# Kernel tuning notes

Measured on AMD Instinct MI355X. Metric: run time of the kernel, lower is better.

The kernel has to match this reference:

```python
import jax, jax.numpy as jnp
import numpy as np

VOXEL_SIZE = jnp.array([0.075, 0.075], dtype=jnp.float32)
PC_RANGE = jnp.array([-54.0, -54.0], dtype=jnp.float32)
FUSION_STRIDE = 8.0
SRC_STRIDES = (4.0, 8.0)
RADII = (2.4, 4.8)
NSAMPLE = 16
NKEY = 500


def _mlp(x, w1, g1, b1, w2, b2):
    # Linear(no bias) + BatchNorm(eval, running mean=0/var=1 -> affine) + ReLU, then Linear
    h = jax.nn.relu((x @ w1) * g1 + b1)
    return h @ w2 + b2


def _world(coords, stride):
    # voxel coord -> world xy center
    return (coords.astype(jnp.float32) + 0.5) * stride * VOXEL_SIZE + PC_RANGE


def _gather_rows(x, idx):
    # x: (B, N, ...), idx: (B, ...) -> per-batch row gather
    return jax.vmap(lambda f, i: f[i])(x, idx)


def _knn(key_world, src_world, src_feat, radius):
    # key_world (B,Nk,2), src_world (B,Ns,2), src_feat (B,Ns,C)
    d2 = jnp.sum((key_world[:, :, None, :] - src_world[:, None, :, :]) ** 2, axis=-1)  # (B,Nk,Ns)
    d2 = jnp.where(d2 <= radius * radius, d2, jnp.inf)
    negd, idx = jax.lax.top_k(-d2, NSAMPLE)  # nearest NSAMPLE within radius, (B,Nk,K)
    valid = jnp.isfinite(negd).astype(src_feat.dtype)  # empty==0 mask
    feats = _gather_rows(src_feat, idx)  # (B,Nk,K,C)
    return feats * valid[..., None]


def setup_inputs() -> dict:
    key = jax.random.key(0)
    ks = jax.random.split(key, 24)
    s = 0.05
    return {
        'fusion_feat': jax.random.normal(ks[0], (2, 20000, 128), jnp.float32),
        'src_feat_a': jax.random.normal(ks[1], (2, 30000, 128), jnp.float32),
        'src_feat_b': jax.random.normal(ks[2], (2, 30000, 128), jnp.float32),
        'heat_w1': jax.random.normal(ks[3], (128, 128), jnp.float32) * s,
        'heat_g1': jnp.ones((128,), jnp.float32),
        'heat_b1': jnp.zeros((128,), jnp.float32),
        'heat_w2': jax.random.normal(ks[4], (128, 10), jnp.float32) * s,
        'heat_b2': jnp.zeros((10,), jnp.float32),
        'knn_w': jax.random.normal(ks[5], (2, 16), jnp.float32) * s,
        'knn_b': jnp.zeros((2,), jnp.float32),
        'kw_w1': jax.random.normal(ks[6], (128, 64), jnp.float32) * s,
        'kw_g1': jnp.ones((64,), jnp.float32),
        'kw_b1': jnp.zeros((64,), jnp.float32),
        'kw_w2': jax.random.normal(ks[7], (64, 3), jnp.float32) * s,
        'kw_b2': jnp.zeros((3,), jnp.float32),
        'fuse_w1': jax.random.normal(ks[8], (256, 256), jnp.float32) * s,
        'fuse_g1': jnp.ones((256,), jnp.float32),
        'fuse_b1': jnp.zeros((256,), jnp.float32),
        'fuse_w2': jax.random.normal(ks[9], (256, 128), jnp.float32) * s,
        'fuse_b2': jnp.zeros((128,), jnp.float32),
        'fusion_coords': jax.random.randint(ks[10], (2, 20000, 2), 0, 180, jnp.int32),
        'src_coords_a': jax.random.randint(ks[11], (2, 30000, 2), 0, 360, jnp.int32),
        'src_coords_b': jax.random.randint(ks[12], (2, 30000, 2), 0, 180, jnp.int32),
    }


def reference(fusion_feat, src_feat_a, src_feat_b, heat_w1, heat_g1, heat_b1,
              heat_w2, heat_b2, knn_w, knn_b, kw_w1, kw_g1, kw_b1, kw_w2, kw_b2,
              fuse_w1, fuse_g1, fuse_b1, fuse_w2, fuse_b2,
              fusion_coords, src_coords_a, src_coords_b):
    B = fusion_feat.shape[0]
    # heatmap head over all fusion voxels
    scores10 = _mlp(fusion_feat, heat_w1, heat_g1, heat_b1, heat_w2, heat_b2)  # (B,Nf,10)
    heat_scores = jnp.max(scores10, axis=-1)
    cls = jnp.argmax(scores10, axis=-1)
    # per-sample top-k key voxel selection
    _, tki = jax.lax.top_k(jax.nn.sigmoid(heat_scores), NKEY)  # (B,Nk)
    key_feat = _gather_rows(fusion_feat, tki)      # (B,Nk,128)
    key_coords = _gather_rows(fusion_coords, tki)  # (B,Nk,2)
    key_class = _gather_rows(cls, tki)             # (B,Nk)
    key_world = _world(key_coords, FUSION_STRIDE)  # (B,Nk,2)

    srcs = ((src_feat_a, src_coords_a), (src_feat_b, src_coords_b))
    mlp_feats = []
    for s, (sf, sc) in enumerate(srcs):
        sw = _world(sc, SRC_STRIDES[s])
        kf = _knn(key_world, sw, sf, RADII[s])  # (B,Nk,K,C), zeroed where empty
        # Linear over the K neighbor axis (knn_feat_mlp: NSAMPLE -> 1)
        mf = jnp.einsum('bnkc,k->bnc', kf, knn_w[s]) + knn_b[s]
        mlp_feats.append(mf)

    w = jax.nn.softmax(_mlp(key_feat, kw_w1, kw_g1, kw_b1, kw_w2, kw_b2), axis=-1)  # (B,Nk,3)
    # faithful to original: key_voxel_feat is re-scaled cumulatively inside the loop
    kvf = key_feat
    fuse_sum = jnp.zeros_like(key_feat)
    for i in range(len(srcs)):
        kvf = w[..., i:i + 1] * kvf
        fuse_sum = fuse_sum + kvf * mlp_feats[i]
    fused = jnp.concatenate([fuse_sum, kvf], axis=-1)  # (B,Nk,256)
    out = _mlp(fused, fuse_w1, fuse_g1, fuse_b1, fuse_w2, fuse_b2)  # (B,Nk,128)

    bs_col = jnp.broadcast_to(jnp.arange(B, dtype=key_coords.dtype)[:, None, None], (B, NKEY, 1))
    key_voxel_indices = jnp.concatenate([bs_col, key_coords], axis=-1).reshape(B * NKEY, 3)
    return (out.reshape(B * NKEY, -1), key_voxel_indices,
            heat_scores.reshape(-1), scores10.reshape(-1, scores10.shape[-1]), key_class)
```

## Files before the change

### kernel.cpp

```cpp
#include <hip/hip_runtime.h>
#include <math.h>

#define BB 2
#define NF 20000
#define NS 30000
#define CH 128
#define NK 500
#define KNN 16
#define KPB 4

#define HA 2.4024f
#define HB 4.8048f
#define NCA 45
#define NCB 23
#define CELLS_A 2025
#define CELLS_B 529

#define GB 8
#define SLICE 3750
#define SLICE4 1875

#define OUT0_OFF 0
#define OUT1_OFF 128000
#define OUT2_OFF 131000
#define OUT3_OFF 171000
#define OUT4_OFF 571000

#define WS_CLS   0
#define WS_TKI   160000
#define WS_KW    164000
#define WS_MF    172000
#define WS_KEYS  WS_MF
#define WS_BH    492000
#define WS_GSTART 1196000
#define WS_PTS    1236880
#define WS_PIDX   2196880

#define STB(s,b)  ((s) ? (4052 + (b) * 530) : ((b) * 2026))

__device__ __forceinline__ void fma4(float4& acc, float sc, const float4& wv) {
    acc.x += sc * wv.x; acc.y += sc * wv.y;
    acc.z += sc * wv.z; acc.w += sc * wv.w;
}

__device__ __forceinline__ unsigned ordf(float s) {
    unsigned u = __float_as_uint(s);
    return (u & 0x80000000u) ? ~u : (u | 0x80000000u);
}

__device__ __forceinline__ int cell_of(int cxi, int cyi, float stride, float inv_h,
                                       int nc, float& sx, float& sy)
{
    sx = __fadd_rn(__fmul_rn(__fmul_rn(__fadd_rn((float)cxi, 0.5f), stride), 0.075f), -54.0f);
    sy = __fadd_rn(__fmul_rn(__fmul_rn(__fadd_rn((float)cyi, 0.5f), stride), 0.075f), -54.0f);
    int cx = (int)floorf((sx + 54.0f) * inv_h);
    int cy = (int)floorf((sy + 54.0f) * inv_h);
    cx = min(max(cx, 0), nc - 1);
    cy = min(max(cy, 0), nc - 1);
    return cy * nc + cx;
}

__global__ __launch_bounds__(256) void heat_kernel(
    const float* __restrict__ x,
    const float* __restrict__ w1,
    const float* __restrict__ g1, const float* __restrict__ b1,
    const float* __restrict__ w2,
    const float* __restrict__ b2,
    float* __restrict__ out_heat,
    float* __restrict__ out_s10,
    int* __restrict__ cls,
    unsigned long long* __restrict__ keys,
    const int* __restrict__ sca, const int* __restrict__ scb,
    int* __restrict__ bh)
{
    __shared__ float As[64 * 72];
    __shared__ float Ws[64 * 132];
    __shared__ float W2s[1280];
    const int tid = threadIdx.x;

    if (blockIdx.x < 4 * GB) {
        const int gflat = blockIdx.x;
        const int sb = gflat >> 3;
        const int gg = gflat & (GB - 1);
        const int s = sb >> 1, b = sb & 1;
        const float stride = s ? 8.0f : 4.0f;
        const float inv_h = s ? (1.0f / HB) : (1.0f / HA);
        const int nc = s ? NCB : NCA;
        const int2* sc = ((const int2*)(s ? scb : sca)) + (size_t)b * NS;
        const int4* scv = (const int4*)sc;
        int* hist = (int*)As;

        for (int i = tid; i < 2048; i += 256) hist[i] = 0;
        __syncthreads();
        for (int p = gg * SLICE4 + tid; p < (gg + 1) * SLICE4; p += 256) {
            int4 v = scv[p];
            float sx, sy;
            int cell0 = cell_of(v.x, v.y, stride, inv_h, nc, sx, sy);
            int cell1 = cell_of(v.z, v.w, stride, inv_h, nc, sx, sy);
            atomicAdd(&hist[cell0], 1);
            atomicAdd(&hist[cell1], 1);
        }
        __syncthreads();
        int* bhp = bh + (gflat << 11);
        for (int i = tid; i < 2048; i += 256) bhp[i] = hist[i];
        return;
    }

    const int m0 = (blockIdx.x - 4 * GB) * 64;
    const int tx = tid & 15;
    const int ty = tid >> 4;

    for (int v = tid; v < 1280; v += 256) W2s[v] = w2[v];

    float acc[4][8];
#pragma unroll
    for (int i = 0; i < 4; ++i)
#pragma unroll
        for (int j = 0; j < 8; ++j) acc[i][j] = 0.f;

    const float4* xv = (const float4*)x;
    const float4* w1v = (const float4*)w1;

    for (int kc = 0; kc < 128; kc += 64) {
#pragma unroll
        for (int i = 0; i < 4; ++i) {
            int v = tid + i * 256;
            int row = v >> 4, c4 = v & 15;
            float4 val = xv[(size_t)(m0 + row) * 32 + (kc >> 2) + c4];
            *(float4*)&As[row * 72 + c4 * 4] = val;
        }
#pragma unroll
        for (int i = 0; i < 8; ++i) {
            int v = tid + i * 256;
            int k = v >> 5, c4 = v & 31;
            float4 val = w1v[(size_t)(kc + k) * 32 + c4];
            *(float4*)&Ws[k * 132 + c4 * 4] = val;
        }
        __syncthreads();

        const float* a0p = &As[(ty * 4 + 0) * 72];
        const float* a1p = &As[(ty * 4 + 1) * 72];
        const float* a2p = &As[(ty * 4 + 2) * 72];
        const float* a3p = &As[(ty * 4 + 3) * 72];
#pragma unroll 4
        for (int k = 0; k < 64; ++k) {
            float4 bA = *(const float4*)&Ws[k * 132 + tx * 8];
            float4 bB = *(const float4*)&Ws[k * 132 + tx * 8 + 4];
            float a0 = a0p[k], a1 = a1p[k], a2 = a2p[k], a3 = a3p[k];
            acc[0][0] += a0 * bA.x; acc[0][1] += a0 * bA.y; acc[0][2] += a0 * bA.z; acc[0][3] += a0 * bA.w;
            acc[0][4] += a0 * bB.x; acc[0][5] += a0 * bB.y; acc[0][6] += a0 * bB.z; acc[0][7] += a0 * bB.w;
            acc[1][0] += a1 * bA.x; acc[1][1] += a1 * bA.y; acc[1][2] += a1 * bA.z; acc[1][3] += a1 * bA.w;
            acc[1][4] += a1 * bB.x; acc[1][5] += a1 * bB.y; acc[1][6] += a1 * bB.z; acc[1][7] += a1 * bB.w;
            acc[2][0] += a2 * bA.x; acc[2][1] += a2 * bA.y; acc[2][2] += a2 * bA.z; acc[2][3] += a2 * bA.w;
            acc[2][4] += a2 * bB.x; acc[2][5] += a2 * bB.y; acc[2][6] += a2 * bB.z; acc[2][7] += a2 * bB.w;
            acc[3][0] += a3 * bA.x; acc[3][1] += a3 * bA.y; acc[3][2] += a3 * bA.z; acc[3][3] += a3 * bA.w;
            acc[3][4] += a3 * bB.x; acc[3][5] += a3 * bB.y; acc[3][6] += a3 * bB.z; acc[3][7] += a3 * bB.w;
        }
        __syncthreads();
    }

    float4 g1a = ((const float4*)g1)[tx * 2], g1b = ((const float4*)g1)[tx * 2 + 1];
    float4 b1a = ((const float4*)b1)[tx * 2], b1b = ((const float4*)b1)[tx * 2 + 1];
    float* Hs = Ws;
#pragma unroll
    for (int i = 0; i < 4; ++i) {
        int row = ty * 4 + i;
        float4 hA, hB;
        hA.x = fmaxf(acc[i][0] * g1a.x + b1a.x, 0.f);
        hA.y = fmaxf(acc[i][1] * g1a.y + b1a.y, 0.f);
        hA.z = fmaxf(acc[i][2] * g1a.z + b1a.z, 0.f);
        hA.w = fmaxf(acc[i][3] * g1a.w + b1a.w, 0.f);
        hB.x = fmaxf(acc[i][4] * g1b.x + b1b.x, 0.f);
        hB.y = fmaxf(acc[i][5] * g1b.y + b1b.y, 0.f);
        hB.z = fmaxf(acc[i][6] * g1b.z + b1b.z, 0.f);
        hB.w = fmaxf(acc[i][7] * g1b.w + b1b.w, 0.f);
        *(float4*)&Hs[row * 132 + tx * 8] = hA;
        *(float4*)&Hs[row * 132 + tx * 8 + 4] = hB;
    }
    __syncthreads();

    const int r = tid >> 2;
    const int p = tid & 3;
    float a2[10];
#pragma unroll
    for (int c = 0; c < 10; ++c) a2[c] = 0.f;
    for (int kk = 0; kk < 32; ++kk) {
        int k = kk * 4 + p;
        float hv = Hs[r * 132 + k];
#pragma unroll
        for (int c = 0; c < 10; ++c) a2[c] += hv * W2s[k * 10 + c];
    }
#pragma unroll
    for (int c = 0; c < 10; ++c) {
        a2[c] += __shfl_xor(a2[c], 1);
        a2[c] += __shfl_xor(a2[c], 2);
    }
    if (p == 0) {
        int m = m0 + r;
        float best = -INFINITY;
        int bi = 0;
#pragma unroll
        for (int c = 0; c < 10; ++c) {
            float s = a2[c] + b2[c];
            out_s10[(size_t)m * 10 + c] = s;
            if (s > best) { best = s; bi = c; }
        }
        out_heat[m] = best;
        cls[m] = bi;
        int b = m / NF;
        unsigned i = (unsigned)(m - b * NF);
        float sig = 1.0f / (1.0f + expf(-best));
        keys[m] = ((unsigned long long)ordf(sig) << 32) | (unsigned)(~i);
    }
}

#define H1BINS 16384

__global__ __launch_bounds__(1024) void mid_kernel(
    const unsigned long long* __restrict__ keys,
    const int* __restrict__ cls,
    const int* __restrict__ fcoords,
    float* __restrict__ out1,
    float* __restrict__ out4,
    int* __restrict__ tki,
    float* __restrict__ keyworld,
    const int* __restrict__ sca, const int* __restrict__ scb,
    const int* __restrict__ bh,
    int* __restrict__ gstart,
    float2* __restrict__ pts, int* __restrict__ pidx)
{
    __shared__ unsigned h[H1BINS];
    __shared__ unsigned sA[1024], sB[1024];
    __shared__ unsigned long long list[1024];
    __shared__ unsigned chunk_s, aboveC_s, T1_s, aboveT1_s, cand_s, thr_s, cnt_s;
    const int tid = threadIdx.x;
    const int blk = blockIdx.x;

    if (blk >= 2) {
        const int idx = blk - 2;
        const int sb = idx >> 3;
        const int j = idx & (GB - 1);
        const int s = sb >> 1, b = sb & 1;
        const int n = s ? CELLS_B : CELLS_A;
        const int nc = s ? NCB : NCA;
        const float stride = s ? 8.0f : 4.0f;
        const float inv_h = s ? (1.0f / HB) : (1.0f / HA);
        const int stb = STB(s, b);
        const int2* sc = ((const int2*)(s ? scb : sca)) + (size_t)b * NS;
        const int4* scv = (const int4*)sc;
        const size_t pbase = ((size_t)s * BB + b) * NS;
        const int* bhsb = bh + (sb << 14);
        int* tot = (int*)h;
        int* cur = ((int*)h) + 2048;
        int* scn0 = (int*)sA;
        int* scn1 = (int*)sB;

        for (int c = tid; c < 2048; c += 1024) {
            int t = 0, pr = 0;
#pragma unroll
            for (int g = 0; g < GB; ++g) {
                int v = bhsb[(g << 11) + c];
                t += v;
                if (g < j) pr += v;
            }
            tot[c] = t;
            cur[c] = pr;
        }
        __syncthreads();
        const int i0 = tid * 2, i1 = tid * 2 + 1;
        int c0 = (i0 < n) ? tot[i0] : 0;
        int c1 = (i1 < n) ? tot[i1] : 0;
        scn0[tid] = c0 + c1;
        __syncthreads();
        int* srcp = scn0; int* dstp = scn1;
        for (int off = 1; off < 1024; off <<= 1) {
            int v = srcp[tid];
            if (tid >= off) v += srcp[tid - off];
            dstp[tid] = v;
            __syncthreads();
            int* t = srcp; srcp = dstp; dstp = t;
        }
        const int excl = (tid == 0) ? 0 : srcp[tid - 1];
        if (i0 < n) {
            if (j == 0) gstart[stb + i0] = excl;
            cur[i0] += excl;
        }
        if (i1 < n) {
            if (j == 0) gstart[stb + i1] = excl + c0;
            cur[i1] += excl + c0;
        }
        if (j == 0 && tid == 0) gstart[stb + n] = NS;
        __syncthreads();
        for (int p = j * SLICE4 + tid; p < (j + 1) * SLICE4; p += 1024) {
            int4 v = scv[p];
            float sx0, sy0, sx1, sy1;
            int cell0 = cell_of(v.x, v.y, stride, inv_h, nc, sx0, sy0);
            int cell1 = cell_of(v.z, v.w, stride, inv_h, nc, sx1, sy1);
            int pos0 = atomicAdd(&cur[cell0], 1);
            int pos1 = atomicAdd(&cur[cell1], 1);
            pts[pbase + pos0] = make_float2(sx0, sy0);
            pidx[pbase + pos0] = p * 2;
            pts[pbase + pos1] = make_float2(sx1, sy1);
            pidx[pbase + pos1] = p * 2 + 1;
        }
        return;
    }

    const int b = blk;
    const unsigned long long* kb = keys + (size_t)b * NF;
    const unsigned K = NK;

    for (int i = tid; i < H1BINS; i += 1024) h[i] = 0u;
    __syncthreads();
#pragma unroll 4
    for (int i = tid; i < NF; i += 1024)
        atomicAdd(&h[(unsigned)(kb[i] >> 50)], 1u);
    __syncthreads();
    unsigned ck = 0;
    {
        int base = tid * 16;
#pragma unroll
        for (int j = 0; j < 16; ++j) ck += h[base + j];
        sA[tid] = ck;
    }
    __syncthreads();
    unsigned* srcp = sA; unsigned* dstp = sB;
    for (int off = 1; off < 1024; off <<= 1) {
        unsigned v = srcp[tid];
        if (tid + off < 1024) v += srcp[tid + off];
        dstp[tid] = v;
        __syncthreads();
        unsigned* t = srcp; srcp = dstp; dstp = t;
    }
    {
        unsigned suf = srcp[tid];
        unsigned above = suf - ck;
        if (above < K && K <= suf) { chunk_s = (unsigned)tid; aboveC_s = above; }
    }
    __syncthreads();
    if (tid == 0) {
        int bin = (int)chunk_s * 16 + 15;
        unsigned acc = aboveC_s;
        for (;; --bin) { if (acc + h[bin] >= K) break; acc += h[bin]; }
        T1_s = (unsigned)bin;
        aboveT1_s = acc;
        cand_s = acc + h[bin];
        cnt_s = 0u;
    }
    __syncthreads();
    const unsigned T1 = T1_s;

    if (cand_s <= 1024u) {
#pragma unroll 4
        for (int i = tid; i < NF; i += 1024) {
            unsigned long long key = kb[i];
            if ((unsigned)(key >> 50) >= T1) {
                unsigned pos = atomicAdd(&cnt_s, 1u);
                if (pos < 1024u) list[pos] = key;
            }
        }
    } else {
        const unsigned K2 = K - aboveT1_s;
        h[tid] = 0u;
        __syncthreads();
#pragma unroll 4
        for (int i = tid; i < NF; i += 1024) {
            unsigned long long key = kb[i];
            if ((unsigned)(key >> 50) == T1)
                atomicAdd(&h[(unsigned)(key >> 40) & 1023u], 1u);
        }
        __syncthreads();
        unsigned hb = h[tid];
        sA[tid] = hb;
        __syncthreads();
        unsigned* s2 = sA; unsigned* d2 = sB;
        for (int off = 1; off < 1024; off <<= 1) {
            unsigned v = s2[tid];
            if (tid + off < 1024) v += s2[tid + off];
            d2[tid] = v;
            __syncthreads();
            unsigned* t = s2; s2 = d2; d2 = t;
        }
        {
            unsigned suf = s2[tid];
            unsigned above = suf - hb;
            if (above < K2 && K2 <= suf) thr_s = (T1 << 10) | (unsigned)tid;
        }
        __syncthreads();
        const unsigned thr24 = thr_s;
#pragma unroll 4
        for (int i = tid; i < NF; i += 1024) {
            unsigned long long key = kb[i];
            if ((unsigned)(key >> 40) >= thr24) {
                unsigned pos = atomicAdd(&cnt_s, 1u);
                if (pos < 1024u) list[pos] = key;
            }
        }
    }
    __syncthreads();
    const int cc = (int)(cnt_s > 1024u ? 1024u : cnt_s);

    if (tid < cc) {
        unsigned long long mykey = list[tid];
        unsigned r = 0;
#pragma unroll 8
        for (int j = 0; j < cc; ++j) r += (list[j] > mykey) ? 1u : 0u;
        if (r < (unsigned)NK) {
            int idx = (int)(~(unsigned)(mykey & 0xFFFFFFFFull));
            tki[b * NK + (int)r] = idx;
            int c0 = fcoords[((size_t)b * NF + idx) * 2 + 0];
            int c1 = fcoords[((size_t)b * NF + idx) * 2 + 1];
            size_t o = (size_t)(b * NK + (int)r);
            out1[o * 3 + 0] = (float)b;
            out1[o * 3 + 1] = (float)c0;
            out1[o * 3 + 2] = (float)c1;
            float wx = __fadd_rn(__fmul_rn(__fmul_rn(__fadd_rn((float)c0, 0.5f), 8.0f), 0.075f), -54.0f);
            float wy = __fadd_rn(__fmul_rn(__fmul_rn(__fadd_rn((float)c1, 0.5f), 8.0f), 0.075f), -54.0f);
            keyworld[o * 2 + 0] = wx;
            keyworld[o * 2 + 1] = wy;
            out4[o] = (float)cls[(size_t)b * NF + idx];
        }
    }
}

__global__ __launch_bounds__(256) void knn_kernel(
    const float* __restrict__ sfa, const float* __restrict__ sfb,
    const int* __restrict__ gstart,
    const float2* __restrict__ pts, const int* __restrict__ pidx,
    const float* __restrict__ knn_w,
    const float* __restrict__ knn_b,
    const float* __restrict__ keyworld,
    float* __restrict__ mf)
{
    __shared__ unsigned long long list[1024];
    __shared__ float psum[128];
    __shared__ unsigned cnt_s;
    const int tid = threadIdx.x;
    const int blk = blockIdx.x;
    const int s = blk / (BB * NK);
    const int rest = blk % (BB * NK);
    const int b = rest / NK;
    const int r = rest % NK;
    const float* sfeat = s ? sfb : sfa;
    const float r2 = s ? (float)(4.8 * 4.8) : (float)(2.4 * 2.4);
    const float inv_h = s ? (1.0f / HB) : (1.0f / HA);
    const int nc = s ? NCB : NCA;
    const int stb = STB(s, b);
    const size_t pbase = ((size_t)s * BB + b) * NS;

    if (tid == 0) cnt_s = 0u;
    __syncthreads();
    const float kx = keyworld[((size_t)b * NK + r) * 2 + 0];
    const float ky = keyworld[((size_t)b * NK + r) * 2 + 1];
    int cx = (int)floorf((kx + 54.0f) * inv_h);
    int cy = (int)floorf((ky + 54.0f) * inv_h);
    cx = min(max(cx, 0), nc - 1);
    cy = min(max(cy, 0), nc - 1);
    const int c0 = max(cx - 1, 0), c1 = min(cx + 1, nc - 1);
    const int cy0 = max(cy - 1, 0), cy1 = min(cy + 1, nc - 1);

    for (int cyy = cy0; cyy <= cy1; ++cyy) {
        int lo = gstart[stb + cyy * nc + c0];
        int hi = gstart[stb + cyy * nc + c1 + 1];
        for (int p = lo + tid; p < hi; p += 256) {
            float2 w = pts[pbase + p];
            float dx = __fsub_rn(kx, w.x);
            float dy = __fsub_rn(ky, w.y);
            float d2 = __fadd_rn(__fmul_rn(dx, dx), __fmul_rn(dy, dy));
            if (d2 <= r2) {
                unsigned pos = atomicAdd(&cnt_s, 1u);
                if (pos < 1024u)
                    list[pos] = ((unsigned long long)__float_as_uint(d2) << 32)
                              | (unsigned)pidx[pbase + p];
            }
        }
    }
    __syncthreads();
    int cc = (int)cnt_s;
    if (cc > 1024) cc = 1024;
    int n2 = 16;
    while (n2 < cc) n2 <<= 1;
    for (int i = tid; i < n2; i += 256)
        if (i >= cc) list[i] = ~0ull;
    __syncthreads();
    for (int kk = 2; kk <= n2; kk <<= 1) {
        for (int j = kk >> 1; j > 0; j >>= 1) {
            for (int i = tid; i < n2; i += 256) {
                int ixj = i ^ j;
                if (ixj > i) {
                    unsigned long long a = list[i], bv = list[ixj];
                    bool up = ((i & kk) == 0);
                    bool sw = up ? (a > bv) : (a < bv);
                    if (sw) { list[i] = bv; list[ixj] = a; }
                }
            }
            __syncthreads();
        }
    }
    {
        int K = cc < KNN ? cc : KNN;
        int col = tid & 127, half = tid >> 7;
        float acc = 0.f;
        int k0 = half * 8, k1 = min(K, half * 8 + 8);
        for (int k = k0; k < k1; ++k) {
            unsigned i = (unsigned)(list[k] & 0xFFFFFFFFull);
            acc += knn_w[s * 16 + k] * sfeat[((size_t)b * NS + i) * CH + col];
        }
        if (half) psum[col] = acc;
        __syncthreads();
        if (!half)
            mf[(((size_t)s * BB + b) * NK + r) * CH + col] = knn_b[s] + acc + psum[col];
    }
}

__global__ __launch_bounds__(1024) void fuse_kernel(
    const float* __restrict__ ffeat,
    const int* __restrict__ tki,
    const float* __restrict__ kw_w1, const float* __restrict__ kw_g1,
    const float* __restrict__ kw_b1, const float* __restrict__ kw_w2,
    const float* __restrict__ kw_b2,
    const float* __restrict__ fuse_w1, const float* __restrict__ fuse_g1,
    const float* __restrict__ fuse_b1, const float* __restrict__ fuse_w2,
    const float* __restrict__ fuse_b2,
    const float* __restrict__ mf,
    float* __restrict__ out0)
{
    __shared__ float pL[16384];
    __shared__ float xsT[512];
    __shared__ float mfs[1024];
    __shared__ float fusedvT[1024];
    __shared__ float h2sT[1024];
    __shared__ float prm[964];
    __shared__ float hsX[256];
    __shared__ float p2[96];
    __shared__ float l3[12];
    __shared__ float wsm[8];
    __shared__ int idxs[KPB], bs[KPB], rs[KPB];
    const int tid = threadIdx.x;
    const int f0 = blockIdx.x * KPB;

    if (tid < 964) {
        float v;
        if (tid < 64)       v = kw_g1[tid];
        else if (tid < 128) v = kw_b1[tid - 64];
        else if (tid < 320) v = kw_w2[tid - 128];
        else if (tid < 323) v = kw_b2[tid - 320];
        else if (tid < 324) v = 0.f;
        else if (tid < 580) v = fuse_g1[tid - 324];
        else if (tid < 836) v = fuse_b1[tid - 580];
        else                v = fuse_b2[tid - 836];
        prm[tid] = v;
    }
    if (tid < KPB) {
        int flat = f0 + tid;
        int b = flat / NK;
        bs[tid] = b;
        rs[tid] = flat - b * NK;
        idxs[tid] = tki[flat];
    }
    __syncthreads();

    if (tid < 128) {
        int key = tid >> 5, c4 = tid & 31;
        float4 v = ((const float4*)(ffeat + ((size_t)bs[key] * NF + idxs[key]) * CH))[c4];
        xsT[(c4 * 4 + 0) * 4 + key] = v.x;
        xsT[(c4 * 4 + 1) * 4 + key] = v.y;
        xsT[(c4 * 4 + 2) * 4 + key] = v.z;
        xsT[(c4 * 4 + 3) * 4 + key] = v.w;
    }
    if (tid < 256) {
        int ss = tid >> 7, key = (tid >> 5) & 3, c4 = tid & 31;
        float4 v = ((const float4*)(mf + (((size_t)ss * BB + bs[key]) * NK + rs[key]) * CH))[c4];
        *(float4*)&mfs[ss * 512 + key * 128 + c4 * 4] = v;
    }
    __syncthreads();

    if (tid < 256) {
        const int og = tid & 15, kseg = tid >> 4;
        float4 wr[8];
#pragma unroll
        for (int m = 0; m < 8; ++m)
            wr[m] = ((const float4*)kw_w1)[(kseg * 8 + m) * 16 + og];
        float4 a0 = {0, 0, 0, 0}, a1 = {0, 0, 0, 0}, a2 = {0, 0, 0, 0}, a3 = {0, 0, 0, 0};
#pragma unroll
        for (int m = 0; m < 8; ++m) {
            float4 f4 = *(const float4*)&xsT[(kseg * 8 + m) * 4];
            fma4(a0, f4.x, wr[m]);
            fma4(a1, f4.y, wr[m]);
            fma4(a2, f4.z, wr[m]);
            fma4(a3, f4.w, wr[m]);
        }
        *(float4*)&pL[(kseg * 4 + 0) * 64 + og * 4] = a0;
        *(float4*)&pL[(kseg * 4 + 1) * 64 + og * 4] = a1;
        *(float4*)&pL[(kseg * 4 + 2) * 64 + og * 4] = a2;
        *(float4*)&pL[(kseg * 4 + 3) * 64 + og * 4] = a3;
    }
    __syncthreads();
    if (tid < 256) {
        int out = tid >> 2, key = tid & 3;
        float s = 0.f;
#pragma unroll
        for (int ks = 0; ks < 16; ++ks) s += pL[(ks * 4 + key) * 64 + out];
        float t = s * prm[out] + prm[64 + out];
        hsX[key * 64 + out] = t > 0.f ? t : 0.f;
    }
    __syncthreads();
    if (tid < 96) {
        int key = tid / 24, rr = tid % 24, out = rr >> 3, seg = rr & 7;
        float acc = 0.f;
#pragma unroll
        for (int m = 0; m < 8; ++m) {
            int k = seg * 8 + m;
            acc += hsX[key * 64 + k] * prm[128 + k * 3 + out];
        }
        p2[(key * 3 + out) * 8 + seg] = acc;
    }
    __syncthreads();
    if (tid < 12) {
        int key = tid / 3, out = tid % 3;
        float s = 0.f;
#pragma unroll
        for (int j = 0; j < 8; ++j) s += p2[(key * 3 + out) * 8 + j];
        l3[key * 3 + out] = s + prm[320 + out];
    }
    __syncthreads();
    if (tid < KPB) {
        float l0 = l3[tid * 3], l1 = l3[tid * 3 + 1], l2 = l3[tid * 3 + 2];
        float m = fmaxf(l0, fmaxf(l1, l2));
        float e0 = expf(l0 - m), e1 = expf(l1 - m), e2 = expf(l2 - m);
        float sum = e0 + e1 + e2;
        wsm[tid * 2 + 0] = e0 / sum;
        wsm[tid * 2 + 1] = e1 / sum;
    }
    __syncthreads();

    {
        int c = tid >> 2, key = tid & 3;
        float w0 = wsm[key * 2], w1_ = wsm[key * 2 + 1];
        float val;
        if (c < 128) {
            float xv_ = xsT[c * 4 + key];
            float m0 = mfs[key * 128 + c];
            float m1 = mfs[512 + key * 128 + c];
            float kv = w0 * xv_;
            float kv2 = w1_ * kv;
            val = kv * m0 + kv2 * m1;
        } else {
            float xv_ = xsT[(c - 128) * 4 + key];
            val = w1_ * (w0 * xv_);
        }
        fusedvT[tid] = val;
    }
    __syncthreads();

    {
        const int og = tid & 63, kseg = tid >> 6;
        const float4* w1v = (const float4*)fuse_w1;
        float4 wr[16];
#pragma unroll
        for (int m = 0; m < 16; ++m)
            wr[m] = w1v[(kseg * 16 + m) * 64 + og];
        float4 a0 = {0, 0, 0, 0}, a1 = {0, 0, 0, 0}, a2 = {0, 0, 0, 0}, a3 = {0, 0, 0, 0};
#pragma unroll
        for (int m = 0; m < 16; ++m) {
            float4 f4 = *(const float4*)&fusedvT[(kseg * 16 + m) * 4];
            fma4(a0, f4.x, wr[m]);
            fma4(a1, f4.y, wr[m]);
            fma4(a2, f4.z, wr[m]);
            fma4(a3, f4.w, wr[m]);
        }
        *(float4*)&pL[(kseg * 4 + 0) * 256 + og * 4] = a0;
        *(float4*)&pL[(kseg * 4 + 1) * 256 + og * 4] = a1;
        *(float4*)&pL[(kseg * 4 + 2) * 256 + og * 4] = a2;
        *(float4*)&pL[(kseg * 4 + 3) * 256 + og * 4] = a3;
    }
    __syncthreads();
    {
        int out = tid >> 2, key = tid & 3;
        float s = 0.f;
#pragma unroll
        for (int ks = 0; ks < 16; ++ks) s += pL[(ks * 4 + key) * 256 + out];
        float t = s * prm[324 + out] + prm[580 + out];
        h2sT[out * 4 + key] = t > 0.f ? t : 0.f;
    }
    __syncthreads();

    {
        const int og2 = tid & 31, kseg2 = tid >> 5;
        const float4* w2v = (const float4*)fuse_w2;
        float4 wr[8];
#pragma unroll
        for (int m = 0; m < 8; ++m)
            wr[m] = w2v[(kseg2 * 8 + m) * 32 + og2];
        float4 a0 = {0, 0, 0, 0}, a1 = {0, 0, 0, 0}, a2 = {0, 0, 0, 0}, a3 = {0, 0, 0, 0};
#pragma unroll
        for (int m = 0; m < 8; ++m) {
            float4 f4 = *(const float4*)&h2sT[(kseg2 * 8 + m) * 4];
            fma4(a0, f4.x, wr[m]);
            fma4(a1, f4.y, wr[m]);
            fma4(a2, f4.z, wr[m]);
            fma4(a3, f4.w, wr[m]);
        }
        *(float4*)&pL[(kseg2 * 4 + 0) * 128 + og2 * 4] = a0;
        *(float4*)&pL[(kseg2 * 4 + 1) * 128 + og2 * 4] = a1;
        *(float4*)&pL[(kseg2 * 4 + 2) * 128 + og2 * 4] = a2;
        *(float4*)&pL[(kseg2 * 4 + 3) * 128 + og2 * 4] = a3;
    }
    __syncthreads();
    if (tid < 512) {
        int out = tid >> 2, key = tid & 3;
        float s = prm[836 + out];
#pragma unroll
        for (int ks = 0; ks < 32; ++ks) s += pL[(ks * 4 + key) * 128 + out];
        out0[((size_t)bs[key] * NK + rs[key]) * CH + out] = s;
    }
}

extern "C" void kernel_launch(void* const* d_in, const int* in_sizes, int n_in,
                              void* d_out, int out_size, void* d_ws, size_t ws_size,
                              hipStream_t stream)
{
    const float* fusion_feat = (const float*)d_in[0];
    const float* src_feat_a  = (const float*)d_in[1];
    const float* src_feat_b  = (const float*)d_in[2];
    const float* heat_w1 = (const float*)d_in[3];
    const float* heat_g1 = (const float*)d_in[4];
    const float* heat_b1 = (const float*)d_in[5];
    const float* heat_w2 = (const float*)d_in[6];
    const float* heat_b2 = (const float*)d_in[7];
    const float* knn_w   = (const float*)d_in[8];
    const float* knn_b   = (const float*)d_in[9];
    const float* kw_w1   = (const float*)d_in[10];
    const float* kw_g1   = (const float*)d_in[11];
    const float* kw_b1   = (const float*)d_in[12];
    const float* kw_w2   = (const float*)d_in[13];
    const float* kw_b2   = (const float*)d_in[14];
    const float* fuse_w1 = (const float*)d_in[15];
    const float* fuse_g1 = (const float*)d_in[16];
    const float* fuse_b1 = (const float*)d_in[17];
    const float* fuse_w2 = (const float*)d_in[18];
    const float* fuse_b2 = (const float*)d_in[19];
    const int* fusion_coords = (const int*)d_in[20];
    const int* src_coords_a  = (const int*)d_in[21];
    const int* src_coords_b  = (const int*)d_in[22];

    float* out = (float*)d_out;
    char* ws = (char*)d_ws;
    int* cls = (int*)(ws + WS_CLS);
    int* tki = (int*)(ws + WS_TKI);
    float* keyworld = (float*)(ws + WS_KW);
    float* mf = (float*)(ws + WS_MF);
    unsigned long long* keys = (unsigned long long*)(ws + WS_KEYS);
    int* bh = (int*)(ws + WS_BH);
    int* gstart = (int*)(ws + WS_GSTART);
    float2* pts = (float2*)(ws + WS_PTS);
    int* pidx = (int*)(ws + WS_PIDX);

    heat_kernel<<<(BB * NF) / 64 + 4 * GB, 256, 0, stream>>>(
        fusion_feat, heat_w1, heat_g1, heat_b1, heat_w2, heat_b2,
        out + OUT2_OFF, out + OUT3_OFF, cls, keys,
        src_coords_a, src_coords_b, bh);

    mid_kernel<<<2 + 4 * GB, 1024, 0, stream>>>(
        keys, cls, fusion_coords,
        out + OUT1_OFF, out + OUT4_OFF, tki, keyworld,
        src_coords_a, src_coords_b, bh, gstart, pts, pidx);

    knn_kernel<<<2 * BB * NK, 256, 0, stream>>>(
        src_feat_a, src_feat_b, gstart, pts, pidx,
        knn_w, knn_b, keyworld, mf);

    fuse_kernel<<<(BB * NK) / KPB, 1024, 0, stream>>>(
        fusion_feat, tki, kw_w1, kw_g1, kw_b1, kw_w2, kw_b2,
        fuse_w1, fuse_g1, fuse_b1, fuse_w2, fuse_b2, mf, out + OUT0_OFF);
}
```

Before: 232.1 us.

## Build top-k histogram in heat kernel and split candidate scan across blocks

The coarse 14-bit score histogram is now accumulated with global atomics in heat_kernel, so mid_kernel no longer rescans all keys to build it. The candidate-collection pass of top-k selection is split across 8 blocks per batch, which append into a global candidate buffer. A last-block-done counter with threadfences picks one block to finish the ranking. This adds a memset, global atomics and a cross-block completion protocol. The fallback path for too many candidates still runs serially in the final block.

New measurement: 328.1 us. 41.4% more time.

```diff
diff --git a/kernel.cpp b/kernel.cpp
--- a/kernel.cpp
+++ b/kernel.cpp
@@ -20,6 +20,9 @@
 #define SLICE 3750
 #define SLICE4 1875
 
+#define TKB 8
+#define TSLICE 2500
+
 #define OUT0_OFF 0
 #define OUT1_OFF 128000
 #define OUT2_OFF 131000
@@ -32,6 +35,10 @@
 #define WS_MF    172000
 #define WS_KEYS  WS_MF
 #define WS_BH    492000
+#define WS_HIST  754144
+#define WS_DONE  885216
+#define WS_CCNT  885224
+#define WS_CAND  885232
 #define WS_GSTART 1196000
 #define WS_PTS    1236880
 #define WS_PIDX   2196880
@@ -71,7 +78,8 @@
     int* __restrict__ cls,
     unsigned long long* __restrict__ keys,
     const int* __restrict__ sca, const int* __restrict__ scb,
-    int* __restrict__ bh)
+    int* __restrict__ bh,
+    unsigned* __restrict__ hist)
 {
     __shared__ float As[64 * 72];
     __shared__ float Ws[64 * 132];
@@ -88,21 +96,21 @@
         const int nc = s ? NCB : NCA;
         const int2* sc = ((const int2*)(s ? scb : sca)) + (size_t)b * NS;
         const int4* scv = (const int4*)sc;
-        int* hist = (int*)As;
-
-        for (int i = tid; i < 2048; i += 256) hist[i] = 0;
+        int* hist_l = (int*)As;
+
+        for (int i = tid; i < 2048; i += 256) hist_l[i] = 0;
         __syncthreads();
         for (int p = gg * SLICE4 + tid; p < (gg + 1) * SLICE4; p += 256) {
             int4 v = scv[p];
             float sx, sy;
             int cell0 = cell_of(v.x, v.y, stride, inv_h, nc, sx, sy);
             int cell1 = cell_of(v.z, v.w, stride, inv_h, nc, sx, sy);
-            atomicAdd(&hist[cell0], 1);
-            atomicAdd(&hist[cell1], 1);
+            atomicAdd(&hist_l[cell0], 1);
+            atomicAdd(&hist_l[cell1], 1);
         }
         __syncthreads();
         int* bhp = bh + (gflat << 11);
-        for (int i = tid; i < 2048; i += 256) bhp[i] = hist[i];
+        for (int i = tid; i < 2048; i += 256) bhp[i] = hist_l[i];
         return;
     }
 
@@ -210,7 +218,9 @@
         int b = m / NF;
         unsigned i = (unsigned)(m - b * NF);
         float sig = 1.0f / (1.0f + expf(-best));
-        keys[m] = ((unsigned long long)ordf(sig) << 32) | (unsigned)(~i);
+        unsigned of = ordf(sig);
+        keys[m] = ((unsigned long long)of << 32) | (unsigned)(~i);
+        atomicAdd(&hist[((size_t)b << 14) + (of >> 18)], 1u);
     }
 }
 
@@ -227,17 +237,22 @@
     const int* __restrict__ sca, const int* __restrict__ scb,
     const int* __restrict__ bh,
     int* __restrict__ gstart,
-    float2* __restrict__ pts, int* __restrict__ pidx)
+    float2* __restrict__ pts, int* __restrict__ pidx,
+    const unsigned* __restrict__ hist,
+    unsigned* __restrict__ ccount,
+    unsigned* __restrict__ done,
+    unsigned long long* __restrict__ candbuf)
 {
     __shared__ unsigned h[H1BINS];
     __shared__ unsigned sA[1024], sB[1024];
     __shared__ unsigned long long list[1024];
     __shared__ unsigned chunk_s, aboveC_s, T1_s, aboveT1_s, cand_s, thr_s, cnt_s;
+    __shared__ unsigned lastflag;
     const int tid = threadIdx.x;
     const int blk = blockIdx.x;
 
-    if (blk >= 2) {
-        const int idx = blk - 2;
+    if (blk >= 2 * TKB) {
+        const int idx = blk - 2 * TKB;
         const int sb = idx >> 3;
         const int j = idx & (GB - 1);
         const int s = sb >> 1, b = sb & 1;
@@ -306,21 +321,18 @@
         return;
     }
 
-    const int b = blk;
+    const int b = blk >> 3;
+    const int j = blk & (TKB - 1);
     const unsigned long long* kb = keys + (size_t)b * NF;
     const unsigned K = NK;
 
-    for (int i = tid; i < H1BINS; i += 1024) h[i] = 0u;
-    __syncthreads();
-#pragma unroll 4
-    for (int i = tid; i < NF; i += 1024)
-        atomicAdd(&h[(unsigned)(kb[i] >> 50)], 1u);
+    for (int i = tid; i < H1BINS; i += 1024) h[i] = hist[((size_t)b << 14) + i];
     __syncthreads();
     unsigned ck = 0;
     {
         int base = tid * 16;
 #pragma unroll
-        for (int j = 0; j < 16; ++j) ck += h[base + j];
+        for (int jj = 0; jj < 16; ++jj) ck += h[base + jj];
         sA[tid] = ck;
     }
     __syncthreads();
@@ -349,16 +361,32 @@
     }
     __syncthreads();
     const unsigned T1 = T1_s;
-
-    if (cand_s <= 1024u) {
-#pragma unroll 4
-        for (int i = tid; i < NF; i += 1024) {
+    const unsigned cand = cand_s;
+
+    if (cand <= 1024u) {
+        for (int i = j * TSLICE + tid; i < (j + 1) * TSLICE; i += 1024) {
             unsigned long long key = kb[i];
             if ((unsigned)(key >> 50) >= T1) {
-                unsigned pos = atomicAdd(&cnt_s, 1u);
-                if (pos < 1024u) list[pos] = key;
+                unsigned pos = atomicAdd(&ccount[b], 1u);
+                candbuf[(b << 10) + pos] = key;
             }
         }
+    }
+    __syncthreads();
+    __threadfence();
+    if (tid == 0) {
+        unsigned old = atomicAdd(&done[b], 1u);
+        lastflag = (old == (unsigned)(TKB - 1)) ? 1u : 0u;
+    }
+    __syncthreads();
+    if (!lastflag) return;
+    __threadfence();
+
+    int cc;
+    if (cand <= 1024u) {
+        cc = (int)cand;
+        for (int i = tid; i < cc; i += 1024) list[i] = candbuf[(b << 10) + i];
+        __syncthreads();
     } else {
         const unsigned K2 = K - aboveT1_s;
         h[tid] = 0u;
@@ -396,15 +424,15 @@
                 if (pos < 1024u) list[pos] = key;
             }
         }
-    }
-    __syncthreads();
-    const int cc = (int)(cnt_s > 1024u ? 1024u : cnt_s);
+        __syncthreads();
+        cc = (int)(cnt_s > 1024u ? 1024u : cnt_s);
+    }
 
     if (tid < cc) {
         unsigned long long mykey = list[tid];
         unsigned r = 0;
 #pragma unroll 8
-        for (int j = 0; j < cc; ++j) r += (list[j] > mykey) ? 1u : 0u;
+        for (int jj = 0; jj < cc; ++jj) r += (list[jj] > mykey) ? 1u : 0u;
         if (r < (unsigned)NK) {
             int idx = (int)(~(unsigned)(mykey & 0xFFFFFFFFull));
             tki[b * NK + (int)r] = idx;
@@ -752,19 +780,26 @@
     float* mf = (float*)(ws + WS_MF);
     unsigned long long* keys = (unsigned long long*)(ws + WS_KEYS);
     int* bh = (int*)(ws + WS_BH);
+    unsigned* hist = (unsigned*)(ws + WS_HIST);
+    unsigned* done = (unsigned*)(ws + WS_DONE);
+    unsigned* ccount = (unsigned*)(ws + WS_CCNT);
+    unsigned long long* candbuf = (unsigned long long*)(ws + WS_CAND);
     int* gstart = (int*)(ws + WS_GSTART);
     float2* pts = (float2*)(ws + WS_PTS);
     int* pidx = (int*)(ws + WS_PIDX);
 
+    hipMemsetAsync(ws + WS_HIST, 0, 131072 + 16, stream);
+
     heat_kernel<<<(BB * NF) / 64 + 4 * GB, 256, 0, stream>>>(
         fusion_feat, heat_w1, heat_g1, heat_b1, heat_w2, heat_b2,
         out + OUT2_OFF, out + OUT3_OFF, cls, keys,
-        src_coords_a, src_coords_b, bh);
-
-    mid_kernel<<<2 + 4 * GB, 1024, 0, stream>>>(
+        src_coords_a, src_coords_b, bh, hist);
+
+    mid_kernel<<<2 * TKB + 4 * GB, 1024, 0, stream>>>(
         keys, cls, fusion_coords,
         out + OUT1_OFF, out + OUT4_OFF, tki, keyworld,
-        src_coords_a, src_coords_b, bh, gstart, pts, pidx);
+        src_coords_a, src_coords_b, bh, gstart, pts, pidx,
+        hist, ccount, done, candbuf);
 
     knn_kernel<<<2 * BB * NK, 256, 0, stream>>>(
         src_feat_a, src_feat_b, gstart, pts, pidx,
```

## Cache top-k histogram bins in LDS and remap heat GEMM columns

Applied to the files above, without the earlier changes.

The top-k selection in mid_kernel now reads the key array once with 128-bit loads and caches each key's 14-bit histogram bin in a 40KB shared-memory ushort array. The candidate pass scans these cached bins instead of re-reading all 64-bit keys from global memory, and fetches a key only when it passes the threshold. In heat_kernel, the A tile row pitch changes from 72 to 76 floats. Each thread's 8 output columns are also split into two groups of 4 spaced 64 apart, so B-tile LDS reads are contiguous across threads and bank conflicts should drop. The extra LDS in mid_kernel may lower occupancy, but only 2 blocks run that path.

Measured after the change: 232.3 us. About the same (+0.1%).

```diff
diff --git a/kernel.cpp b/kernel.cpp
--- a/kernel.cpp
+++ b/kernel.cpp
@@ -73,7 +73,7 @@
     const int* __restrict__ sca, const int* __restrict__ scb,
     int* __restrict__ bh)
 {
-    __shared__ float As[64 * 72];
+    __shared__ float As[64 * 76];
     __shared__ float Ws[64 * 132];
     __shared__ float W2s[1280];
     const int tid = threadIdx.x;
@@ -88,21 +88,21 @@
         const int nc = s ? NCB : NCA;
         const int2* sc = ((const int2*)(s ? scb : sca)) + (size_t)b * NS;
         const int4* scv = (const int4*)sc;
-        int* hist = (int*)As;
-
-        for (int i = tid; i < 2048; i += 256) hist[i] = 0;
+        int* hist_l = (int*)As;
+
+        for (int i = tid; i < 2048; i += 256) hist_l[i] = 0;
         __syncthreads();
         for (int p = gg * SLICE4 + tid; p < (gg + 1) * SLICE4; p += 256) {
             int4 v = scv[p];
             float sx, sy;
             int cell0 = cell_of(v.x, v.y, stride, inv_h, nc, sx, sy);
             int cell1 = cell_of(v.z, v.w, stride, inv_h, nc, sx, sy);
-            atomicAdd(&hist[cell0], 1);
-            atomicAdd(&hist[cell1], 1);
+            atomicAdd(&hist_l[cell0], 1);
+            atomicAdd(&hist_l[cell1], 1);
         }
         __syncthreads();
         int* bhp = bh + (gflat << 11);
-        for (int i = tid; i < 2048; i += 256) bhp[i] = hist[i];
+        for (int i = tid; i < 2048; i += 256) bhp[i] = hist_l[i];
         return;
     }
 
@@ -127,7 +127,7 @@
             int v = tid + i * 256;
             int row = v >> 4, c4 = v & 15;
             float4 val = xv[(size_t)(m0 + row) * 32 + (kc >> 2) + c4];
-            *(float4*)&As[row * 72 + c4 * 4] = val;
+            *(float4*)&As[row * 76 + c4 * 4] = val;
         }
 #pragma unroll
         for (int i = 0; i < 8; ++i) {
@@ -138,14 +138,14 @@
         }
         __syncthreads();
 
-        const float* a0p = &As[(ty * 4 + 0) * 72];
-        const float* a1p = &As[(ty * 4 + 1) * 72];
-        const float* a2p = &As[(ty * 4 + 2) * 72];
-        const float* a3p = &As[(ty * 4 + 3) * 72];
+        const float* a0p = &As[(ty * 4 + 0) * 76];
+        const float* a1p = &As[(ty * 4 + 1) * 76];
+        const float* a2p = &As[(ty * 4 + 2) * 76];
+        const float* a3p = &As[(ty * 4 + 3) * 76];
 #pragma unroll 4
         for (int k = 0; k < 64; ++k) {
-            float4 bA = *(const float4*)&Ws[k * 132 + tx * 8];
-            float4 bB = *(const float4*)&Ws[k * 132 + tx * 8 + 4];
+            float4 bA = *(const float4*)&Ws[k * 132 + tx * 4];
+            float4 bB = *(const float4*)&Ws[k * 132 + 64 + tx * 4];
             float a0 = a0p[k], a1 = a1p[k], a2 = a2p[k], a3 = a3p[k];
             acc[0][0] += a0 * bA.x; acc[0][1] += a0 * bA.y; acc[0][2] += a0 * bA.z; acc[0][3] += a0 * bA.w;
             acc[0][4] += a0 * bB.x; acc[0][5] += a0 * bB.y; acc[0][6] += a0 * bB.z; acc[0][7] += a0 * bB.w;
@@ -159,8 +159,8 @@
         __syncthreads();
     }
 
-    float4 g1a = ((const float4*)g1)[tx * 2], g1b = ((const float4*)g1)[tx * 2 + 1];
-    float4 b1a = ((const float4*)b1)[tx * 2], b1b = ((const float4*)b1)[tx * 2 + 1];
+    float4 g1a = ((const float4*)g1)[tx], g1b = ((const float4*)g1)[16 + tx];
+    float4 b1a = ((const float4*)b1)[tx], b1b = ((const float4*)b1)[16 + tx];
     float* Hs = Ws;
 #pragma unroll
     for (int i = 0; i < 4; ++i) {
@@ -174,8 +174,8 @@
         hB.y = fmaxf(acc[i][5] * g1b.y + b1b.y, 0.f);
         hB.z = fmaxf(acc[i][6] * g1b.z + b1b.z, 0.f);
         hB.w = fmaxf(acc[i][7] * g1b.w + b1b.w, 0.f);
-        *(float4*)&Hs[row * 132 + tx * 8] = hA;
-        *(float4*)&Hs[row * 132 + tx * 8 + 4] = hB;
+        *(float4*)&Hs[row * 132 + tx * 4] = hA;
+        *(float4*)&Hs[row * 132 + 64 + tx * 4] = hB;
     }
     __syncthreads();
 
@@ -232,6 +232,7 @@
     __shared__ unsigned h[H1BINS];
     __shared__ unsigned sA[1024], sB[1024];
     __shared__ unsigned long long list[1024];
+    __shared__ unsigned short bins16[NF];
     __shared__ unsigned chunk_s, aboveC_s, T1_s, aboveT1_s, cand_s, thr_s, cnt_s;
     const int tid = threadIdx.x;
     const int blk = blockIdx.x;
@@ -312,9 +313,15 @@
 
     for (int i = tid; i < H1BINS; i += 1024) h[i] = 0u;
     __syncthreads();
-#pragma unroll 4
-    for (int i = tid; i < NF; i += 1024)
-        atomicAdd(&h[(unsigned)(kb[i] >> 50)], 1u);
+    for (int i2 = tid; i2 < NF / 2; i2 += 1024) {
+        ulonglong2 kv = ((const ulonglong2*)kb)[i2];
+        unsigned b0 = (unsigned)(kv.x >> 50);
+        unsigned b1_ = (unsigned)(kv.y >> 50);
+        bins16[2 * i2] = (unsigned short)b0;
+        bins16[2 * i2 + 1] = (unsigned short)b1_;
+        atomicAdd(&h[b0], 1u);
+        atomicAdd(&h[b1_], 1u);
+    }
     __syncthreads();
     unsigned ck = 0;
     {
@@ -351,12 +358,16 @@
     const unsigned T1 = T1_s;
 
     if (cand_s <= 1024u) {
-#pragma unroll 4
-        for (int i = tid; i < NF; i += 1024) {
-            unsigned long long key = kb[i];
-            if ((unsigned)(key >> 50) >= T1) {
+        const unsigned* b32v = (const unsigned*)bins16;
+        for (int i2 = tid; i2 < NF / 2; i2 += 1024) {
+            unsigned pk = b32v[i2];
+            if ((pk & 0xFFFFu) >= T1) {
                 unsigned pos = atomicAdd(&cnt_s, 1u);
-                if (pos < 1024u) list[pos] = key;
+                if (pos < 1024u) list[pos] = kb[2 * i2];
+            }
+            if ((pk >> 16) >= T1) {
+                unsigned pos = atomicAdd(&cnt_s, 1u);
+                if (pos < 1024u) list[pos] = kb[2 * i2 + 1];
             }
         }
     } else {
```
